# Performance work log

Measured on AMD Instinct MI355X. Metric: run time of the kernel, lower is better.

The kernel has to match this reference:

```python
import jax, jax.numpy as jnp
import numpy as np

VOCAB, EMB, HID, OUT = 50257, 512, 512, 2
B, T = 64, 1024

def setup_inputs() -> dict:
    key = jax.random.key(0)
    ks = jax.random.split(key, 8)
    s_e = 1.0 / np.sqrt(EMB)
    s_h = 1.0 / np.sqrt(HID)
    return {
        "x": jax.random.randint(ks[0], (B, T), 0, VOCAB, dtype=jnp.int64),
        "emb": jax.random.normal(ks[1], (VOCAB, EMB), jnp.float32) * 0.02,
        "w_ih": jax.random.uniform(ks[2], (4 * HID, EMB), jnp.float32, -s_h, s_h),
        "w_hh": jax.random.uniform(ks[3], (4 * HID, HID), jnp.float32, -s_h, s_h),
        "b_ih": jax.random.uniform(ks[4], (4 * HID,), jnp.float32, -s_h, s_h),
        "b_hh": jax.random.uniform(ks[5], (4 * HID,), jnp.float32, -s_h, s_h),
        "w_out": jax.random.uniform(ks[6], (OUT, HID), jnp.float32, -s_h, s_h),
        "b_out": jax.random.uniform(ks[7], (OUT,), jnp.float32, -s_h, s_h),
    }

def _lstm_last_hidden(e, w_ih, w_hh, b_ih, b_hh):
    # e: [B, T, E]. Precompute input projection for all timesteps (one big GEMM).
    Bc, Tc, _ = e.shape
    H = w_hh.shape[1]
    x_proj = jnp.einsum('bte,ge->btg', e, w_ih) + b_ih + b_hh  # [B, T, 4H]
    x_proj = jnp.transpose(x_proj, (1, 0, 2))                   # [T, B, 4H]

    def step(carry, xt):
        h, c = carry
        gates = xt + h @ w_hh.T                 # [B, 4H]
        i, f, g, o = jnp.split(gates, 4, axis=-1)  # PyTorch gate order i,f,g,o
        i = jax.nn.sigmoid(i)
        f = jax.nn.sigmoid(f)
        g = jnp.tanh(g)
        o = jax.nn.sigmoid(o)
        c = f * c + i * g
        h = o * jnp.tanh(c)
        return (h, c), None

    h0 = jnp.zeros((Bc, H), e.dtype)
    c0 = jnp.zeros((Bc, H), e.dtype)
    (h_last, _), _ = jax.lax.scan(step, (h0, c0), x_proj)
    return h_last  # [B, H] == output at last timestep

def reference(x, emb, w_ih, w_hh, b_ih, b_hh, w_out, b_out):
    e = emb[x]                                   # [B, T, E] embedding lookup
    h_last = _lstm_last_hidden(e, w_ih, w_hh, b_ih, b_hh)
    out = h_last @ w_out.T + b_out               # [B, OUT]
    return jnp.squeeze(out)
```

## Files before the change

### kernel.cpp

```cpp
#include <hip/hip_runtime.h>
#include <hip/hip_bf16.h>
#include <stdint.h>

typedef __bf16   bf16x8 __attribute__((ext_vector_type(8)));
typedef float    f32x4  __attribute__((ext_vector_type(4)));
typedef float    fl4    __attribute__((ext_vector_type(4)));
typedef uint32_t u32;
typedef unsigned long long u64;
typedef uint32_t u32x4  __attribute__((ext_vector_type(4)));

#define T_    1024
#define G4H   2048

__device__ __forceinline__ float bf2f(uint16_t b){
  u32 u = ((u32)b) << 16; float f; __builtin_memcpy(&f, &u, 4); return f;
}
__device__ __forceinline__ uint16_t f2bf(float f){
  u32 u; __builtin_memcpy(&u, &f, 4);
  u = u + 0x7fffu + ((u >> 16) & 1u);
  return (uint16_t)(u >> 16);
}
__device__ __forceinline__ float fsig(float x){ return 1.f / (1.f + __expf(-x)); }
__device__ __forceinline__ float ftanh(float x){
  float xc = fminf(fmaxf(x, -15.f), 15.f);
  float e  = __expf(2.f * xc);
  return (e - 1.f) / (e + 1.f);
}
__device__ __forceinline__ void gl_lds16(const void* g, void* l){
  __builtin_amdgcn_global_load_lds((const __attribute__((address_space(1))) void*)g,
                                   (__attribute__((address_space(3))) void*)l, 16, 0, 0);
}
__device__ __forceinline__ u32 umaxv(u32 a, u32 b){ return a > b ? a : b; }

__global__ void detect_i64(const u32* __restrict__ x, u32* __restrict__ flag){
  int gid = blockIdx.x * 256 + threadIdx.x;
  u32 v = x[1 + 2 * gid];
  if (v != 0u) atomicOr(flag, 1u);
}

__global__ __launch_bounds__(256) void gather_embed(
    const u32* __restrict__ x, const float* __restrict__ emb,
    uint16_t* __restrict__ e, const u32* __restrict__ flag){
  int row = blockIdx.x * 8 + (threadIdx.x >> 5);
  int c0  = (threadIdx.x & 31) * 16;
  u32 tok = (*flag != 0u) ? x[row] : x[2 * row];
  const float* s = emb + (size_t)tok * 512 + c0;
  fl4 a = *(const fl4*)(s);
  fl4 b = *(const fl4*)(s + 4);
  fl4 c = *(const fl4*)(s + 8);
  fl4 d = *(const fl4*)(s + 12);
  u32x4 q0 = { (u32)f2bf(a.x) | ((u32)f2bf(a.y) << 16),
               (u32)f2bf(a.z) | ((u32)f2bf(a.w) << 16),
               (u32)f2bf(b.x) | ((u32)f2bf(b.y) << 16),
               (u32)f2bf(b.z) | ((u32)f2bf(b.w) << 16) };
  u32x4 q1 = { (u32)f2bf(c.x) | ((u32)f2bf(c.y) << 16),
               (u32)f2bf(c.z) | ((u32)f2bf(c.w) << 16),
               (u32)f2bf(d.x) | ((u32)f2bf(d.y) << 16),
               (u32)f2bf(d.z) | ((u32)f2bf(d.w) << 16) };
  *(u32x4*)(e + (size_t)row * 512 + c0)     = q0;
  *(u32x4*)(e + (size_t)row * 512 + c0 + 8) = q1;
}

__global__ __launch_bounds__(256) void prep_w(
    const float* __restrict__ w_ih, const float* __restrict__ w_hh,
    const float* __restrict__ b_ih, const float* __restrict__ b_hh,
    uint16_t* __restrict__ wih, uint16_t* __restrict__ whi,
    uint16_t* __restrict__ wlo, float* __restrict__ bias){
  int bidx = blockIdx.x, t = threadIdx.x;
  if (bidx < 512){
    size_t i0 = (size_t)bidx * 2048 + t * 8;
    fl4 a = *(const fl4*)(w_ih + i0), b = *(const fl4*)(w_ih + i0 + 4);
    u32x4 q = { (u32)f2bf(a.x) | ((u32)f2bf(a.y) << 16),
                (u32)f2bf(a.z) | ((u32)f2bf(a.w) << 16),
                (u32)f2bf(b.x) | ((u32)f2bf(b.y) << 16),
                (u32)f2bf(b.z) | ((u32)f2bf(b.w) << 16) };
    *(u32x4*)(wih + i0) = q;
  } else if (bidx < 1024){
    size_t i0 = (size_t)(bidx - 512) * 2048 + t * 8;
    fl4 a = *(const fl4*)(w_hh + i0), b = *(const fl4*)(w_hh + i0 + 4);
    float v[8] = {a.x,a.y,a.z,a.w,b.x,b.y,b.z,b.w};
    uint16_t hi[8], lo[8];
    #pragma unroll
    for (int j = 0; j < 8; ++j){
      hi[j] = f2bf(v[j]);
      lo[j] = f2bf(v[j] - bf2f(hi[j]));
    }
    u32x4 qh = { (u32)hi[0]|((u32)hi[1]<<16), (u32)hi[2]|((u32)hi[3]<<16),
                 (u32)hi[4]|((u32)hi[5]<<16), (u32)hi[6]|((u32)hi[7]<<16) };
    u32x4 ql = { (u32)lo[0]|((u32)lo[1]<<16), (u32)lo[2]|((u32)lo[3]<<16),
                 (u32)lo[4]|((u32)lo[5]<<16), (u32)lo[6]|((u32)lo[7]<<16) };
    *(u32x4*)(whi + i0) = qh;
    *(u32x4*)(wlo + i0) = ql;
  } else {
    int i0 = t * 8;
    #pragma unroll
    for (int j = 0; j < 8; ++j) bias[i0 + j] = b_ih[i0 + j] + b_hh[i0 + j];
  }
}

__global__ __launch_bounds__(256,1) void gemm_xproj(
    const uint16_t* __restrict__ A, const uint16_t* __restrict__ Bw,
    uint16_t* __restrict__ C){
  __shared__ uint16_t As[128 * 64];
  __shared__ uint16_t Bs[128 * 64];
  int m0 = blockIdx.x * 128, n0 = blockIdx.y * 128;
  int tid = threadIdx.x, wid = tid >> 6, l = tid & 63;
  int wm = (wid >> 1) * 64, wn = (wid & 1) * 64;
  f32x4 zz = {0.f, 0.f, 0.f, 0.f};
  f32x4 acc[4][4];
  #pragma unroll
  for (int i = 0; i < 4; ++i)
    #pragma unroll
    for (int j = 0; j < 4; ++j) acc[i][j] = zz;
  const uint16_t* Ap = A  + (size_t)m0 * 512;
  const uint16_t* Bp = Bw + (size_t)n0 * 512;
  for (int kt = 0; kt < 8; ++kt){
    __syncthreads();
    #pragma unroll
    for (int i = 0; i < 4; ++i){
      int c = (i * 4 + wid) * 64 + l;
      int row = c >> 3, col = c & 7;
      int scol = col ^ (row & 7);
      gl_lds16(Ap + (size_t)row * 512 + kt * 64 + scol * 8, &As[c * 8]);
      gl_lds16(Bp + (size_t)row * 512 + kt * 64 + scol * 8, &Bs[c * 8]);
    }
    __syncthreads();
    #pragma unroll
    for (int kk = 0; kk < 2; ++kk){
      bf16x8 af[4], bfr[4];
      #pragma unroll
      for (int i = 0; i < 4; ++i){
        int ra = wm + i * 16 + (l & 15);
        int rb = wn + i * 16 + (l & 15);
        int ci = kk * 4 + (l >> 4);
        af[i]  = *(const bf16x8*)((const char*)As + (size_t)ra * 128 + ((ci ^ (ra & 7)) << 4));
        bfr[i] = *(const bf16x8*)((const char*)Bs + (size_t)rb * 128 + ((ci ^ (rb & 7)) << 4));
      }
      #pragma unroll
      for (int mi = 0; mi < 4; ++mi)
        #pragma unroll
        for (int ni = 0; ni < 4; ++ni)
          acc[mi][ni] = __builtin_amdgcn_mfma_f32_16x16x32_bf16(af[mi], bfr[ni], acc[mi][ni], 0, 0, 0);
    }
  }
  #pragma unroll
  for (int mi = 0; mi < 4; ++mi)
    #pragma unroll
    for (int ni = 0; ni < 4; ++ni)
      #pragma unroll
      for (int r = 0; r < 4; ++r){
        int m = m0 + wm + mi * 16 + (l >> 4) * 4 + r;
        int n = n0 + wn + ni * 16 + (l & 15);
        C[(size_t)m * 2048 + n] = f2bf(acc[mi][ni][r]);
      }
}

__global__ __launch_bounds__(256,1) void lstm_rec(
    const uint16_t* __restrict__ xp, const uint16_t* __restrict__ whi,
    const uint16_t* __restrict__ wlo, const float* __restrict__ bias,
    u32* __restrict__ hbuf){
  int bid = blockIdx.x;
  int g = bid & 3;
  int slice = bid >> 2;
  int tid = threadIdx.x, wid = tid >> 6, l = tid & 63;
  int n_local = wid * 16 + (l & 15);
  int u = slice * 16 + (n_local >> 2);
  int gate = n_local & 3;
  int grow = gate * 512 + u;
  int bquad = (l >> 4) * 4;

  bf16x8 Bhi[16], Blo[16];
  {
    const uint16_t* ph = whi + (size_t)grow * 512 + (l >> 4) * 8;
    const uint16_t* pl = wlo + (size_t)grow * 512 + (l >> 4) * 8;
    #pragma unroll
    for (int ks = 0; ks < 16; ++ks){
      Bhi[ks] = *(const bf16x8*)(ph + ks * 32);
      Blo[ks] = *(const bf16x8*)(pl + ks * 32);
    }
  }
  float biasr = bias[grow];
  float c_[4] = {0.f, 0.f, 0.f, 0.f};
  __shared__ uint16_t hhi[16 * 512];
  __shared__ uint16_t hlo[16 * 512];
  u32* hb0 = hbuf + (size_t)(g * 2 + 0) * (16 * 512);
  u32* hb1 = hbuf + (size_t)(g * 2 + 1) * (16 * 512);
  const uint16_t* xpb = xp + (size_t)(g * 16 + bquad) * T_ * G4H + grow;
  int alive = 1000000;
  int sb = tid & 15;
  int sc = tid >> 4;
  int ssig = (sb & 7) ^ ((sb >> 3) << 2);
  int brow = l & 15;
  int rsig = (brow & 7) ^ ((brow >> 3) << 2);

  for (int t = 0; t < T_; ++t){
    uint16_t xpr[4];
    #pragma unroll
    for (int r = 0; r < 4; ++r)
      xpr[r] = xpb[(size_t)r * T_ * G4H + (size_t)t * G4H];
    if (t > 0){
      const u32* hrow = ((t & 1) ? hb0 : hb1) + sb * 512 + sc * 32;
      u64 av = (u64)(uintptr_t)hrow;
      u32 eoffc = (u32)(((t - 1) >> 1) & 1) << 30;
      for (;;){
        u32 s0, s1;
        asm volatile(
          "global_load_dword %0, %2, off sc0 sc1\n\t"
          "global_load_dword %1, %2, off offset:64 sc0 sc1\n\t"
          "s_waitcnt vmcnt(0)"
          : "=&v"(s0), "=&v"(s1) : "v"(av) : "memory");
        u32 wa = (s0 - eoffc) & 0x7fffffffu;
        u32 wb = (s1 - eoffc) & 0x7fffffffu;
        if (umaxv(wa, wb) < 0x3f810000u) break;
        if (--alive < 0) break;
      }
      u32x4 q0, q1, q2, q3, q4, q5, q6, q7;
      for (;;){
        asm volatile(
          "global_load_dwordx4 %0, %8, off sc0 sc1\n\t"
          "global_load_dwordx4 %1, %8, off offset:16 sc0 sc1\n\t"
          "global_load_dwordx4 %2, %8, off offset:32 sc0 sc1\n\t"
          "global_load_dwordx4 %3, %8, off offset:48 sc0 sc1\n\t"
          "global_load_dwordx4 %4, %8, off offset:64 sc0 sc1\n\t"
          "global_load_dwordx4 %5, %8, off offset:80 sc0 sc1\n\t"
          "global_load_dwordx4 %6, %8, off offset:96 sc0 sc1\n\t"
          "global_load_dwordx4 %7, %8, off offset:112 sc0 sc1\n\t"
          "s_waitcnt vmcnt(0)"
          : "=&v"(q0), "=&v"(q1), "=&v"(q2), "=&v"(q3),
            "=&v"(q4), "=&v"(q5), "=&v"(q6), "=&v"(q7)
          : "v"(av) : "memory");
        u32 m = 0;
        #define VQ(Q) \
          m = umaxv(m, umaxv((Q.x - eoffc) & 0x7fffffffu, (Q.y - eoffc) & 0x7fffffffu)); \
          m = umaxv(m, umaxv((Q.z - eoffc) & 0x7fffffffu, (Q.w - eoffc) & 0x7fffffffu));
        VQ(q0) VQ(q1) VQ(q2) VQ(q3) VQ(q4) VQ(q5) VQ(q6) VQ(q7)
        #undef VQ
        if (m < 0x3f810000u) break;
        if (--alive < 0) break;
      }
      u32 V[32];
      *(u32x4*)&V[0]  = q0; *(u32x4*)&V[4]  = q1;
      *(u32x4*)&V[8]  = q2; *(u32x4*)&V[12] = q3;
      *(u32x4*)&V[16] = q4; *(u32x4*)&V[20] = q5;
      *(u32x4*)&V[24] = q6; *(u32x4*)&V[28] = q7;
      u32 H[16], L[16];
      #pragma unroll
      for (int j = 0; j < 16; ++j){
        u32 a = V[2*j] - eoffc, b = V[2*j+1] - eoffc;
        H[j] = (a >> 16)      | (b & 0xffff0000u);
        L[j] = (a & 0xffffu)  | (b << 16);
      }
      #pragma unroll
      for (int cc = 0; cc < 4; ++cc){
        int slot = (sc * 4 + cc) ^ ssig;
        u32x4 qh = {H[4*cc], H[4*cc+1], H[4*cc+2], H[4*cc+3]};
        u32x4 ql = {L[4*cc], L[4*cc+1], L[4*cc+2], L[4*cc+3]};
        *(u32x4*)((char*)hhi + sb * 1024 + slot * 16) = qh;
        *(u32x4*)((char*)hlo + sb * 1024 + slot * 16) = ql;
      }
    }
    __syncthreads();
    f32x4 acc = {0.f, 0.f, 0.f, 0.f};
    if (t > 0){
      #pragma unroll
      for (int ks = 0; ks < 16; ++ks){
        int slot = (ks * 4 + (l >> 4)) ^ rsig;
        bf16x8 ah = *(const bf16x8*)((const char*)hhi + brow * 1024 + slot * 16);
        bf16x8 al = *(const bf16x8*)((const char*)hlo + brow * 1024 + slot * 16);
        acc = __builtin_amdgcn_mfma_f32_16x16x32_bf16(ah, Bhi[ks], acc, 0, 0, 0);
        acc = __builtin_amdgcn_mfma_f32_16x16x32_bf16(al, Bhi[ks], acc, 0, 0, 0);
        acc = __builtin_amdgcn_mfma_f32_16x16x32_bf16(ah, Blo[ks], acc, 0, 0, 0);
      }
    }
    float hn[4];
    int qb = l & ~3;
    #pragma unroll
    for (int r = 0; r < 4; ++r){
      float pre = acc[r] + bf2f(xpr[r]) + biasr;
      float gi = __shfl(pre, qb + 0, 64);
      float gf = __shfl(pre, qb + 1, 64);
      float gg = __shfl(pre, qb + 2, 64);
      float go = __shfl(pre, qb + 3, 64);
      float i_ = fsig(gi), f_ = fsig(gf), g_ = ftanh(gg), o_ = fsig(go);
      c_[r] = f_ * c_[r] + i_ * g_;
      hn[r] = o_ * ftanh(c_[r]);
    }
    if ((l & 3) == 0){
      u32 eoffp = (u32)((t >> 1) & 1) << 30;
      u32* dst = ((t & 1) ? hb1 : hb0) + u;
      #pragma unroll
      for (int r = 0; r < 4; ++r){
        uint16_t hi = f2bf(hn[r]);
        uint16_t lo = f2bf(hn[r] - bf2f(hi));
        u32 packed = (((u32)hi << 16) | (u32)lo) + eoffp;
        __hip_atomic_store(dst + (size_t)(bquad + r) * 512, packed,
                           __ATOMIC_RELAXED, __HIP_MEMORY_SCOPE_AGENT);
      }
    }
    __syncthreads();
  }
}

__global__ void final_proj(const u32* __restrict__ hbuf, const float* __restrict__ w_out,
                           const float* __restrict__ b_out, float* __restrict__ out){
  int b = blockIdx.x;
  int g = b >> 4, bl = b & 15;
  const u32* hp = hbuf + (size_t)(g * 2 + 1) * (16 * 512) + bl * 512;
  int tid = threadIdx.x;
  float p0 = 0.f, p1 = 0.f;
  #pragma unroll
  for (int j = 0; j < 8; ++j){
    int k = tid * 8 + j;
    u32 pk = hp[k] - 0x40000000u;
    float h = bf2f((uint16_t)(pk >> 16)) + bf2f((uint16_t)(pk & 0xffffu));
    p0 += h * w_out[k];
    p1 += h * w_out[512 + k];
  }
  #pragma unroll
  for (int off = 32; off > 0; off >>= 1){
    p0 += __shfl_down(p0, off, 64);
    p1 += __shfl_down(p1, off, 64);
  }
  if (tid == 0){
    out[b * 2 + 0] = p0 + b_out[0];
    out[b * 2 + 1] = p1 + b_out[1];
  }
}

extern "C" void kernel_launch(void* const* d_in, const int* in_sizes, int n_in,
                              void* d_out, int out_size, void* d_ws, size_t ws_size,
                              hipStream_t stream){
  const u32*   x     = (const u32*)d_in[0];
  const float* emb   = (const float*)d_in[1];
  const float* w_ih  = (const float*)d_in[2];
  const float* w_hh  = (const float*)d_in[3];
  const float* b_ih  = (const float*)d_in[4];
  const float* b_hh  = (const float*)d_in[5];
  const float* w_out = (const float*)d_in[6];
  const float* b_out = (const float*)d_in[7];
  char* ws = (char*)d_ws;

  uint16_t* e     = (uint16_t*)(ws);
  uint16_t* xp    = (uint16_t*)(ws + 67108864ull);
  uint16_t* wih   = (uint16_t*)(ws + 335544320ull);
  uint16_t* whi   = (uint16_t*)(ws + 337641472ull);
  uint16_t* wlo   = (uint16_t*)(ws + 339738624ull);
  float*    bias  = (float*)   (ws + 341835776ull);
  u32*      flagw = (u32*)     (ws + 341843968ull);
  u32*      hbuf  = (u32*)     (ws + 341901312ull);

  hipMemsetAsync(flagw, 0, 4, stream);
  hipMemsetAsync(hbuf, 0xBF, 4ull * 8 * 16 * 512, stream);
  detect_i64  <<<128, 256, 0, stream>>>(x, flagw);
  gather_embed<<<8192, 256, 0, stream>>>(x, emb, e, flagw);
  prep_w      <<<1025, 256, 0, stream>>>(w_ih, w_hh, b_ih, b_hh, wih, whi, wlo, bias);
  gemm_xproj  <<<dim3(512, 16), 256, 0, stream>>>(e, wih, xp);
  lstm_rec    <<<128, 256, 0, stream>>>(xp, whi, wlo, bias, hbuf);
  final_proj  <<<64, 64, 0, stream>>>(hbuf, w_out, b_out, (float*)d_out);
}
```

Before: 4.841 ms.

## Replace per-thread h polling with per-wave flag counters and split MFMA accumulators

```diff
diff --git a/kernel.cpp b/kernel.cpp
--- a/kernel.cpp
+++ b/kernel.cpp
@@ -158,7 +158,7 @@
 __global__ __launch_bounds__(256,1) void lstm_rec(
     const uint16_t* __restrict__ xp, const uint16_t* __restrict__ whi,
     const uint16_t* __restrict__ wlo, const float* __restrict__ bias,
-    u32* __restrict__ hbuf){
+    u32* __restrict__ hbuf, u32* __restrict__ flags){
   int bid = blockIdx.x;
   int g = bid & 3;
   int slice = bid >> 2;
@@ -185,11 +185,10 @@
   __shared__ uint16_t hlo[16 * 512];
   u32* hb0 = hbuf + (size_t)(g * 2 + 0) * (16 * 512);
   u32* hb1 = hbuf + (size_t)(g * 2 + 1) * (16 * 512);
+  u32* flagg = flags + g * 128;
   const uint16_t* xpb = xp + (size_t)(g * 16 + bquad) * T_ * G4H + grow;
   int alive = 1000000;
-  int sb = tid & 15;
-  int sc = tid >> 4;
-  int ssig = (sb & 7) ^ ((sb >> 3) << 2);
+  int pb_base = wid;
   int brow = l & 15;
   int rsig = (brow & 7) ^ ((brow >> 3) << 2);
 
@@ -199,36 +198,41 @@
     for (int r = 0; r < 4; ++r)
       xpr[r] = xpb[(size_t)r * T_ * G4H + (size_t)t * G4H];
     if (t > 0){
-      const u32* hrow = ((t & 1) ? hb0 : hb1) + sb * 512 + sc * 32;
-      u64 av = (u64)(uintptr_t)hrow;
+      if (wid == 0){
+        u64 fa = (u64)(uintptr_t)(flagg + l);
+        for (;;){
+          u32 f0, f1;
+          asm volatile(
+            "global_load_dword %0, %2, off sc0 sc1\n\t"
+            "global_load_dword %1, %2, off offset:256 sc0 sc1\n\t"
+            "s_waitcnt vmcnt(0)"
+            : "=&v"(f0), "=&v"(f1) : "v"(fa) : "memory");
+          if (__all(((int)(f0 - (u32)t) >= 0) && ((int)(f1 - (u32)t) >= 0))) break;
+          if (--alive < 0) break;
+        }
+      }
+    }
+    __syncthreads();
+    if (t > 0){
+      const char* hb = (const char*)((t & 1) ? hb0 : hb1);
+      u64 a0 = (u64)(uintptr_t)(hb + tid * 32);
+      u64 a1 = a0 + 8192, a2 = a0 + 16384, a3 = a0 + 24576;
       u32 eoffc = (u32)(((t - 1) >> 1) & 1) << 30;
-      for (;;){
-        u32 s0, s1;
-        asm volatile(
-          "global_load_dword %0, %2, off sc0 sc1\n\t"
-          "global_load_dword %1, %2, off offset:64 sc0 sc1\n\t"
-          "s_waitcnt vmcnt(0)"
-          : "=&v"(s0), "=&v"(s1) : "v"(av) : "memory");
-        u32 wa = (s0 - eoffc) & 0x7fffffffu;
-        u32 wb = (s1 - eoffc) & 0x7fffffffu;
-        if (umaxv(wa, wb) < 0x3f810000u) break;
-        if (--alive < 0) break;
-      }
       u32x4 q0, q1, q2, q3, q4, q5, q6, q7;
       for (;;){
         asm volatile(
           "global_load_dwordx4 %0, %8, off sc0 sc1\n\t"
           "global_load_dwordx4 %1, %8, off offset:16 sc0 sc1\n\t"
-          "global_load_dwordx4 %2, %8, off offset:32 sc0 sc1\n\t"
-          "global_load_dwordx4 %3, %8, off offset:48 sc0 sc1\n\t"
-          "global_load_dwordx4 %4, %8, off offset:64 sc0 sc1\n\t"
-          "global_load_dwordx4 %5, %8, off offset:80 sc0 sc1\n\t"
-          "global_load_dwordx4 %6, %8, off offset:96 sc0 sc1\n\t"
-          "global_load_dwordx4 %7, %8, off offset:112 sc0 sc1\n\t"
+          "global_load_dwordx4 %2, %9, off sc0 sc1\n\t"
+          "global_load_dwordx4 %3, %9, off offset:16 sc0 sc1\n\t"
+          "global_load_dwordx4 %4, %10, off sc0 sc1\n\t"
+          "global_load_dwordx4 %5, %10, off offset:16 sc0 sc1\n\t"
+          "global_load_dwordx4 %6, %11, off sc0 sc1\n\t"
+          "global_load_dwordx4 %7, %11, off offset:16 sc0 sc1\n\t"
           "s_waitcnt vmcnt(0)"
           : "=&v"(q0), "=&v"(q1), "=&v"(q2), "=&v"(q3),
             "=&v"(q4), "=&v"(q5), "=&v"(q6), "=&v"(q7)
-          : "v"(av) : "memory");
+          : "v"(a0), "v"(a1), "v"(a2), "v"(a3) : "memory");
         u32 m = 0;
         #define VQ(Q) \
           m = umaxv(m, umaxv((Q.x - eoffc) & 0x7fffffffu, (Q.y - eoffc) & 0x7fffffffu)); \
@@ -237,40 +241,47 @@
         #undef VQ
         if (m < 0x3f810000u) break;
         if (--alive < 0) break;
+        __builtin_amdgcn_s_sleep(1);
       }
       u32 V[32];
       *(u32x4*)&V[0]  = q0; *(u32x4*)&V[4]  = q1;
       *(u32x4*)&V[8]  = q2; *(u32x4*)&V[12] = q3;
       *(u32x4*)&V[16] = q4; *(u32x4*)&V[20] = q5;
       *(u32x4*)&V[24] = q6; *(u32x4*)&V[28] = q7;
-      u32 H[16], L[16];
-      #pragma unroll
-      for (int j = 0; j < 16; ++j){
-        u32 a = V[2*j] - eoffc, b = V[2*j+1] - eoffc;
-        H[j] = (a >> 16)      | (b & 0xffff0000u);
-        L[j] = (a & 0xffffu)  | (b << 16);
-      }
-      #pragma unroll
-      for (int cc = 0; cc < 4; ++cc){
-        int slot = (sc * 4 + cc) ^ ssig;
-        u32x4 qh = {H[4*cc], H[4*cc+1], H[4*cc+2], H[4*cc+3]};
-        u32x4 ql = {L[4*cc], L[4*cc+1], L[4*cc+2], L[4*cc+3]};
-        *(u32x4*)((char*)hhi + sb * 1024 + slot * 16) = qh;
-        *(u32x4*)((char*)hlo + sb * 1024 + slot * 16) = ql;
+      #pragma unroll
+      for (int j = 0; j < 4; ++j){
+        int b = 4 * j + pb_base;
+        int ssig = (b & 7) ^ ((b >> 3) << 2);
+        int slot = l ^ ssig;
+        u32 H[4], L[4];
+        #pragma unroll
+        for (int i = 0; i < 4; ++i){
+          u32 a = V[8*j + 2*i]     - eoffc;
+          u32 bb = V[8*j + 2*i + 1] - eoffc;
+          H[i] = (a >> 16)     | (bb & 0xffff0000u);
+          L[i] = (a & 0xffffu) | (bb << 16);
+        }
+        u32x4 qh = {H[0], H[1], H[2], H[3]};
+        u32x4 ql = {L[0], L[1], L[2], L[3]};
+        *(u32x4*)((char*)hhi + b * 1024 + slot * 16) = qh;
+        *(u32x4*)((char*)hlo + b * 1024 + slot * 16) = ql;
       }
     }
     __syncthreads();
     f32x4 acc = {0.f, 0.f, 0.f, 0.f};
     if (t > 0){
+      f32x4 accA = {0.f,0.f,0.f,0.f}, accB = accA, accC = accA;
       #pragma unroll
       for (int ks = 0; ks < 16; ++ks){
         int slot = (ks * 4 + (l >> 4)) ^ rsig;
         bf16x8 ah = *(const bf16x8*)((const char*)hhi + brow * 1024 + slot * 16);
         bf16x8 al = *(const bf16x8*)((const char*)hlo + brow * 1024 + slot * 16);
-        acc = __builtin_amdgcn_mfma_f32_16x16x32_bf16(ah, Bhi[ks], acc, 0, 0, 0);
-        acc = __builtin_amdgcn_mfma_f32_16x16x32_bf16(al, Bhi[ks], acc, 0, 0, 0);
-        acc = __builtin_amdgcn_mfma_f32_16x16x32_bf16(ah, Blo[ks], acc, 0, 0, 0);
-      }
+        accA = __builtin_amdgcn_mfma_f32_16x16x32_bf16(ah, Bhi[ks], accA, 0, 0, 0);
+        accB = __builtin_amdgcn_mfma_f32_16x16x32_bf16(al, Bhi[ks], accB, 0, 0, 0);
+        accC = __builtin_amdgcn_mfma_f32_16x16x32_bf16(ah, Blo[ks], accC, 0, 0, 0);
+      }
+      #pragma unroll
+      for (int i = 0; i < 4; ++i) acc[i] = (accA[i] + accB[i]) + accC[i];
     }
     float hn[4];
     int qb = l & ~3;
@@ -285,19 +296,19 @@
       c_[r] = f_ * c_[r] + i_ * g_;
       hn[r] = o_ * ftanh(c_[r]);
     }
-    if ((l & 3) == 0){
+    {
+      int r = l & 3;
       u32 eoffp = (u32)((t >> 1) & 1) << 30;
-      u32* dst = ((t & 1) ? hb1 : hb0) + u;
-      #pragma unroll
-      for (int r = 0; r < 4; ++r){
-        uint16_t hi = f2bf(hn[r]);
-        uint16_t lo = f2bf(hn[r] - bf2f(hi));
-        u32 packed = (((u32)hi << 16) | (u32)lo) + eoffp;
-        __hip_atomic_store(dst + (size_t)(bquad + r) * 512, packed,
-                           __ATOMIC_RELAXED, __HIP_MEMORY_SCOPE_AGENT);
-      }
-    }
-    __syncthreads();
+      uint16_t hi = f2bf(hn[r]);
+      uint16_t lo = f2bf(hn[r] - bf2f(hi));
+      u32 packed = (((u32)hi << 16) | (u32)lo) + eoffp;
+      u32* dst = ((t & 1) ? hb1 : hb0) + (size_t)(bquad + r) * 512 + u;
+      __hip_atomic_store(dst, packed, __ATOMIC_RELAXED, __HIP_MEMORY_SCOPE_AGENT);
+    }
+    asm volatile("s_waitcnt vmcnt(0)" ::: "memory");
+    if (l == 0)
+      __hip_atomic_store(flagg + slice * 4 + wid, (u32)(t + 1),
+                         __ATOMIC_RELAXED, __HIP_MEMORY_SCOPE_AGENT);
   }
 }
 
@@ -348,13 +359,15 @@
   float*    bias  = (float*)   (ws + 341835776ull);
   u32*      flagw = (u32*)     (ws + 341843968ull);
   u32*      hbuf  = (u32*)     (ws + 341901312ull);
+  u32*      flags = (u32*)     (ws + 342163456ull);
 
   hipMemsetAsync(flagw, 0, 4, stream);
+  hipMemsetAsync(flags, 0, 4 * 128 * 4, stream);
   hipMemsetAsync(hbuf, 0xBF, 4ull * 8 * 16 * 512, stream);
   detect_i64  <<<128, 256, 0, stream>>>(x, flagw);
   gather_embed<<<8192, 256, 0, stream>>>(x, emb, e, flagw);
   prep_w      <<<1025, 256, 0, stream>>>(w_ih, w_hh, b_ih, b_hh, wih, whi, wlo, bias);
   gemm_xproj  <<<dim3(512, 16), 256, 0, stream>>>(e, wih, xp);
-  lstm_rec    <<<128, 256, 0, stream>>>(xp, whi, wlo, bias, hbuf);
+  lstm_rec    <<<128, 256, 0, stream>>>(xp, whi, wlo, bias, hbuf, flags);
   final_proj  <<<64, 64, 0, stream>>>(hbuf, w_out, b_out, (float*)d_out);
 }
```

After: 4.946 ms. +2.2%, slower.

## Streamline LSTM recurrence step: optimistic h load, split MFMA chains, per-lane gate activations

Applied to the files above, without the earlier changes.

```diff
diff --git a/kernel.cpp b/kernel.cpp
--- a/kernel.cpp
+++ b/kernel.cpp
@@ -192,6 +192,7 @@
   int ssig = (sb & 7) ^ ((sb >> 3) << 2);
   int brow = l & 15;
   int rsig = (brow & 7) ^ ((brow >> 3) << 2);
+  bool isg = (gate == 2);
 
   for (int t = 0; t < T_; ++t){
     uint16_t xpr[4];
@@ -202,42 +203,63 @@
       const u32* hrow = ((t & 1) ? hb0 : hb1) + sb * 512 + sc * 32;
       u64 av = (u64)(uintptr_t)hrow;
       u32 eoffc = (u32)(((t - 1) >> 1) & 1) << 30;
-      for (;;){
-        u32 s0, s1;
-        asm volatile(
-          "global_load_dword %0, %2, off sc0 sc1\n\t"
-          "global_load_dword %1, %2, off offset:64 sc0 sc1\n\t"
-          "s_waitcnt vmcnt(0)"
-          : "=&v"(s0), "=&v"(s1) : "v"(av) : "memory");
-        u32 wa = (s0 - eoffc) & 0x7fffffffu;
-        u32 wb = (s1 - eoffc) & 0x7fffffffu;
-        if (umaxv(wa, wb) < 0x3f810000u) break;
-        if (--alive < 0) break;
-      }
       u32x4 q0, q1, q2, q3, q4, q5, q6, q7;
-      for (;;){
-        asm volatile(
-          "global_load_dwordx4 %0, %8, off sc0 sc1\n\t"
-          "global_load_dwordx4 %1, %8, off offset:16 sc0 sc1\n\t"
-          "global_load_dwordx4 %2, %8, off offset:32 sc0 sc1\n\t"
-          "global_load_dwordx4 %3, %8, off offset:48 sc0 sc1\n\t"
-          "global_load_dwordx4 %4, %8, off offset:64 sc0 sc1\n\t"
-          "global_load_dwordx4 %5, %8, off offset:80 sc0 sc1\n\t"
-          "global_load_dwordx4 %6, %8, off offset:96 sc0 sc1\n\t"
-          "global_load_dwordx4 %7, %8, off offset:112 sc0 sc1\n\t"
-          "s_waitcnt vmcnt(0)"
-          : "=&v"(q0), "=&v"(q1), "=&v"(q2), "=&v"(q3),
-            "=&v"(q4), "=&v"(q5), "=&v"(q6), "=&v"(q7)
-          : "v"(av) : "memory");
-        u32 m = 0;
-        #define VQ(Q) \
-          m = umaxv(m, umaxv((Q.x - eoffc) & 0x7fffffffu, (Q.y - eoffc) & 0x7fffffffu)); \
-          m = umaxv(m, umaxv((Q.z - eoffc) & 0x7fffffffu, (Q.w - eoffc) & 0x7fffffffu));
-        VQ(q0) VQ(q1) VQ(q2) VQ(q3) VQ(q4) VQ(q5) VQ(q6) VQ(q7)
-        #undef VQ
-        if (m < 0x3f810000u) break;
-        if (--alive < 0) break;
-      }
+      u32 m;
+      #define LOAD8() \
+        asm volatile( \
+          "global_load_dwordx4 %0, %8, off sc0 sc1\n\t" \
+          "global_load_dwordx4 %1, %8, off offset:16 sc0 sc1\n\t" \
+          "global_load_dwordx4 %2, %8, off offset:32 sc0 sc1\n\t" \
+          "global_load_dwordx4 %3, %8, off offset:48 sc0 sc1\n\t" \
+          "global_load_dwordx4 %4, %8, off offset:64 sc0 sc1\n\t" \
+          "global_load_dwordx4 %5, %8, off offset:80 sc0 sc1\n\t" \
+          "global_load_dwordx4 %6, %8, off offset:96 sc0 sc1\n\t" \
+          "global_load_dwordx4 %7, %8, off offset:112 sc0 sc1\n\t" \
+          "s_waitcnt vmcnt(0)" \
+          : "=&v"(q0), "=&v"(q1), "=&v"(q2), "=&v"(q3), \
+            "=&v"(q4), "=&v"(q5), "=&v"(q6), "=&v"(q7) \
+          : "v"(av) : "memory")
+      #define VAL8() do{ m = 0; \
+        { u32x4 QQ; \
+          QQ=q0; m=umaxv(m,umaxv((QQ.x-eoffc)&0x7fffffffu,(QQ.y-eoffc)&0x7fffffffu)); \
+                 m=umaxv(m,umaxv((QQ.z-eoffc)&0x7fffffffu,(QQ.w-eoffc)&0x7fffffffu)); \
+          QQ=q1; m=umaxv(m,umaxv((QQ.x-eoffc)&0x7fffffffu,(QQ.y-eoffc)&0x7fffffffu)); \
+                 m=umaxv(m,umaxv((QQ.z-eoffc)&0x7fffffffu,(QQ.w-eoffc)&0x7fffffffu)); \
+          QQ=q2; m=umaxv(m,umaxv((QQ.x-eoffc)&0x7fffffffu,(QQ.y-eoffc)&0x7fffffffu)); \
+                 m=umaxv(m,umaxv((QQ.z-eoffc)&0x7fffffffu,(QQ.w-eoffc)&0x7fffffffu)); \
+          QQ=q3; m=umaxv(m,umaxv((QQ.x-eoffc)&0x7fffffffu,(QQ.y-eoffc)&0x7fffffffu)); \
+                 m=umaxv(m,umaxv((QQ.z-eoffc)&0x7fffffffu,(QQ.w-eoffc)&0x7fffffffu)); \
+          QQ=q4; m=umaxv(m,umaxv((QQ.x-eoffc)&0x7fffffffu,(QQ.y-eoffc)&0x7fffffffu)); \
+                 m=umaxv(m,umaxv((QQ.z-eoffc)&0x7fffffffu,(QQ.w-eoffc)&0x7fffffffu)); \
+          QQ=q5; m=umaxv(m,umaxv((QQ.x-eoffc)&0x7fffffffu,(QQ.y-eoffc)&0x7fffffffu)); \
+                 m=umaxv(m,umaxv((QQ.z-eoffc)&0x7fffffffu,(QQ.w-eoffc)&0x7fffffffu)); \
+          QQ=q6; m=umaxv(m,umaxv((QQ.x-eoffc)&0x7fffffffu,(QQ.y-eoffc)&0x7fffffffu)); \
+                 m=umaxv(m,umaxv((QQ.z-eoffc)&0x7fffffffu,(QQ.w-eoffc)&0x7fffffffu)); \
+          QQ=q7; m=umaxv(m,umaxv((QQ.x-eoffc)&0x7fffffffu,(QQ.y-eoffc)&0x7fffffffu)); \
+                 m=umaxv(m,umaxv((QQ.z-eoffc)&0x7fffffffu,(QQ.w-eoffc)&0x7fffffffu)); \
+        } }while(0)
+      LOAD8(); VAL8();
+      if (m >= 0x3f810000u){
+        for (;;){
+          u32 s0, s1;
+          asm volatile(
+            "global_load_dword %0, %2, off sc0 sc1\n\t"
+            "global_load_dword %1, %2, off offset:64 sc0 sc1\n\t"
+            "s_waitcnt vmcnt(0)"
+            : "=&v"(s0), "=&v"(s1) : "v"(av) : "memory");
+          u32 wa = (s0 - eoffc) & 0x7fffffffu;
+          u32 wb = (s1 - eoffc) & 0x7fffffffu;
+          if (umaxv(wa, wb) < 0x3f810000u) break;
+          if (--alive < 0) break;
+        }
+        for (;;){
+          LOAD8(); VAL8();
+          if (m < 0x3f810000u) break;
+          if (--alive < 0) break;
+        }
+      }
+      #undef LOAD8
+      #undef VAL8
       u32 V[32];
       *(u32x4*)&V[0]  = q0; *(u32x4*)&V[4]  = q1;
       *(u32x4*)&V[8]  = q2; *(u32x4*)&V[12] = q3;
@@ -262,40 +284,49 @@
     __syncthreads();
     f32x4 acc = {0.f, 0.f, 0.f, 0.f};
     if (t > 0){
+      f32x4 accA = {0.f,0.f,0.f,0.f}, accB = accA, accC = accA;
       #pragma unroll
       for (int ks = 0; ks < 16; ++ks){
         int slot = (ks * 4 + (l >> 4)) ^ rsig;
         bf16x8 ah = *(const bf16x8*)((const char*)hhi + brow * 1024 + slot * 16);
         bf16x8 al = *(const bf16x8*)((const char*)hlo + brow * 1024 + slot * 16);
-        acc = __builtin_amdgcn_mfma_f32_16x16x32_bf16(ah, Bhi[ks], acc, 0, 0, 0);
-        acc = __builtin_amdgcn_mfma_f32_16x16x32_bf16(al, Bhi[ks], acc, 0, 0, 0);
-        acc = __builtin_amdgcn_mfma_f32_16x16x32_bf16(ah, Blo[ks], acc, 0, 0, 0);
-      }
+        accA = __builtin_amdgcn_mfma_f32_16x16x32_bf16(ah, Bhi[ks], accA, 0, 0, 0);
+        accB = __builtin_amdgcn_mfma_f32_16x16x32_bf16(al, Bhi[ks], accB, 0, 0, 0);
+        accC = __builtin_amdgcn_mfma_f32_16x16x32_bf16(ah, Blo[ks], accC, 0, 0, 0);
+      }
+      #pragma unroll
+      for (int i = 0; i < 4; ++i) acc[i] = (accA[i] + accB[i]) + accC[i];
+    }
+    float y[4];
+    #pragma unroll
+    for (int r = 0; r < 4; ++r){
+      float pre = acc[r] + bf2f(xpr[r]) + biasr;
+      float a2 = isg ? 2.f * pre : pre;
+      a2 = fminf(fmaxf(a2, -30.f), 30.f);
+      float e = __expf(-a2);
+      float num = isg ? (1.f - e) : 1.f;
+      y[r] = num / (1.f + e);
     }
     float hn[4];
     int qb = l & ~3;
     #pragma unroll
     for (int r = 0; r < 4; ++r){
-      float pre = acc[r] + bf2f(xpr[r]) + biasr;
-      float gi = __shfl(pre, qb + 0, 64);
-      float gf = __shfl(pre, qb + 1, 64);
-      float gg = __shfl(pre, qb + 2, 64);
-      float go = __shfl(pre, qb + 3, 64);
-      float i_ = fsig(gi), f_ = fsig(gf), g_ = ftanh(gg), o_ = fsig(go);
-      c_[r] = f_ * c_[r] + i_ * g_;
-      hn[r] = o_ * ftanh(c_[r]);
-    }
-    if ((l & 3) == 0){
+      float yi = __shfl(y[r], qb + 0, 64);
+      float yf = __shfl(y[r], qb + 1, 64);
+      float yg = __shfl(y[r], qb + 2, 64);
+      float yo = __shfl(y[r], qb + 3, 64);
+      c_[r] = yf * c_[r] + yi * yg;
+      hn[r] = yo * ftanh(c_[r]);
+    }
+    {
+      int r = l & 3;
       u32 eoffp = (u32)((t >> 1) & 1) << 30;
-      u32* dst = ((t & 1) ? hb1 : hb0) + u;
-      #pragma unroll
-      for (int r = 0; r < 4; ++r){
-        uint16_t hi = f2bf(hn[r]);
-        uint16_t lo = f2bf(hn[r] - bf2f(hi));
-        u32 packed = (((u32)hi << 16) | (u32)lo) + eoffp;
-        __hip_atomic_store(dst + (size_t)(bquad + r) * 512, packed,
-                           __ATOMIC_RELAXED, __HIP_MEMORY_SCOPE_AGENT);
-      }
+      float hsel = (l & 2) ? ((l & 1) ? hn[3] : hn[2]) : ((l & 1) ? hn[1] : hn[0]);
+      uint16_t hi  = f2bf(hsel);
+      uint16_t lo2 = f2bf(hsel - bf2f(hi));
+      u32 packed = (((u32)hi << 16) | (u32)lo2) + eoffp;
+      u32* dst = ((t & 1) ? hb1 : hb0) + (size_t)(bquad + r) * 512 + u;
+      __hip_atomic_store(dst, packed, __ATOMIC_RELAXED, __HIP_MEMORY_SCOPE_AGENT);
     }
     __syncthreads();
   }
```

Result: slower. 5.610 ms (+15.9%).

## Split MFMA accumulators, evaluate gate nonlinearities pre-shuffle, vectorize hidden-state stores

Applied to the files above, without the earlier changes.

```diff
diff --git a/kernel.cpp b/kernel.cpp
--- a/kernel.cpp
+++ b/kernel.cpp
@@ -192,6 +192,9 @@
   int ssig = (sb & 7) ^ ((sb >> 3) << 2);
   int brow = l & 15;
   int rsig = (brow & 7) ^ ((brow >> 3) << 2);
+  bool isg = (gate == 2);
+  int ubase = slice * 16 + wid * 4;
+  int rsel = (l & 15) >> 2;
 
   for (int t = 0; t < T_; ++t){
     uint16_t xpr[4];
@@ -262,39 +265,57 @@
     __syncthreads();
     f32x4 acc = {0.f, 0.f, 0.f, 0.f};
     if (t > 0){
+      f32x4 accA = {0.f,0.f,0.f,0.f}, accB = accA, accC = accA;
       #pragma unroll
       for (int ks = 0; ks < 16; ++ks){
         int slot = (ks * 4 + (l >> 4)) ^ rsig;
         bf16x8 ah = *(const bf16x8*)((const char*)hhi + brow * 1024 + slot * 16);
         bf16x8 al = *(const bf16x8*)((const char*)hlo + brow * 1024 + slot * 16);
-        acc = __builtin_amdgcn_mfma_f32_16x16x32_bf16(ah, Bhi[ks], acc, 0, 0, 0);
-        acc = __builtin_amdgcn_mfma_f32_16x16x32_bf16(al, Bhi[ks], acc, 0, 0, 0);
-        acc = __builtin_amdgcn_mfma_f32_16x16x32_bf16(ah, Blo[ks], acc, 0, 0, 0);
-      }
+        accA = __builtin_amdgcn_mfma_f32_16x16x32_bf16(ah, Bhi[ks], accA, 0, 0, 0);
+        accB = __builtin_amdgcn_mfma_f32_16x16x32_bf16(al, Bhi[ks], accB, 0, 0, 0);
+        accC = __builtin_amdgcn_mfma_f32_16x16x32_bf16(ah, Blo[ks], accC, 0, 0, 0);
+      }
+      #pragma unroll
+      for (int i = 0; i < 4; ++i) acc[i] = (accA[i] + accB[i]) + accC[i];
+    }
+    float y[4];
+    #pragma unroll
+    for (int r = 0; r < 4; ++r){
+      float pre = acc[r] + bf2f(xpr[r]) + biasr;
+      float a2 = isg ? 2.f * pre : pre;
+      a2 = fminf(fmaxf(a2, -30.f), 30.f);
+      float e = __expf(-a2);
+      float num = isg ? (1.f - e) : 1.f;
+      y[r] = num / (1.f + e);
     }
     float hn[4];
     int qb = l & ~3;
     #pragma unroll
     for (int r = 0; r < 4; ++r){
-      float pre = acc[r] + bf2f(xpr[r]) + biasr;
-      float gi = __shfl(pre, qb + 0, 64);
-      float gf = __shfl(pre, qb + 1, 64);
-      float gg = __shfl(pre, qb + 2, 64);
-      float go = __shfl(pre, qb + 3, 64);
-      float i_ = fsig(gi), f_ = fsig(gf), g_ = ftanh(gg), o_ = fsig(go);
-      c_[r] = f_ * c_[r] + i_ * g_;
-      hn[r] = o_ * ftanh(c_[r]);
-    }
-    if ((l & 3) == 0){
+      float yi = __shfl(y[r], qb + 0, 64);
+      float yf = __shfl(y[r], qb + 1, 64);
+      float yg = __shfl(y[r], qb + 2, 64);
+      float yo = __shfl(y[r], qb + 3, 64);
+      c_[r] = yf * c_[r] + yi * yg;
+      hn[r] = yo * ftanh(c_[r]);
+    }
+    {
       u32 eoffp = (u32)((t >> 1) & 1) << 30;
-      u32* dst = ((t & 1) ? hb1 : hb0) + u;
-      #pragma unroll
-      for (int r = 0; r < 4; ++r){
-        uint16_t hi = f2bf(hn[r]);
-        uint16_t lo = f2bf(hn[r] - bf2f(hi));
-        u32 packed = (((u32)hi << 16) | (u32)lo) + eoffp;
-        __hip_atomic_store(dst + (size_t)(bquad + r) * 512, packed,
-                           __ATOMIC_RELAXED, __HIP_MEMORY_SCOPE_AGENT);
+      float hv = (l & 2) ? ((l & 1) ? hn[3] : hn[2]) : ((l & 1) ? hn[1] : hn[0]);
+      uint16_t hi  = f2bf(hv);
+      uint16_t lo2 = f2bf(hv - bf2f(hi));
+      u32 p = (((u32)hi << 16) | (u32)lo2) + eoffp;
+      int sbase = (l & 48) | rsel;
+      u32 v0 = __shfl(p, sbase + 0,  64);
+      u32 v1 = __shfl(p, sbase + 4,  64);
+      u32 v2 = __shfl(p, sbase + 8,  64);
+      u32 v3 = __shfl(p, sbase + 12, 64);
+      if ((l & 3) == 0){
+        int row = bquad + rsel;
+        u64 daddr = (u64)(uintptr_t)(((t & 1) ? hb1 : hb0) + (size_t)row * 512 + ubase);
+        u32x4 val = {v0, v1, v2, v3};
+        asm volatile("global_store_dwordx4 %0, %1, off sc0 sc1"
+                     :: "v"(daddr), "v"(val) : "memory");
       }
     }
     __syncthreads();
```

New measurement: 4.881 ms. Within noise of the previous version (+0.8%).
